# Kernel tuning notes

Hardware: AMD Instinct MI355X
Metric: run time of the kernel (lower is better)

## Reference

```python
import jax, jax.numpy as jnp
import numpy as np

EPS = 1e-10
PHI = (1.0 + np.sqrt(5.0)) / 2.0
TAU = 2.0 * np.pi
LOG_CUTOFF = float(np.log(PHI ** 2))  # log(lambda_cutoff)


def _log_abs_diff(la, lb, same_sign):
    # log|a - b| (same sign) or log(|a| + |b|) (opposite sign), all in log space
    hi = jnp.maximum(la, lb)
    lo = jnp.minimum(la, lb)
    d = jnp.minimum(lo - hi, -1e-7)  # guard log1p(-1) on the (masked) diagonal
    log_diff = hi + jnp.log1p(-jnp.exp(d))
    log_sum = jnp.logaddexp(la, lb)
    return jnp.where(same_sign, log_diff, log_sum)


def log_cartesian_distance(ell1, theta1, ell2, theta2):
    # elementwise / broadcasting version of compute_log_cartesian_distance
    cos1, sin1 = jnp.cos(theta1), jnp.sin(theta1)
    cos2, sin2 = jnp.cos(theta2), jnp.sin(theta2)
    lx1 = ell1 + jnp.log(jnp.abs(cos1) + EPS)
    ly1 = ell1 + jnp.log(jnp.abs(sin1) + EPS)
    lx2 = ell2 + jnp.log(jnp.abs(cos2) + EPS)
    ly2 = ell2 + jnp.log(jnp.abs(sin2) + EPS)
    same_x = (jnp.sign(cos1) * jnp.sign(cos2)) > 0
    same_y = (jnp.sign(sin1) * jnp.sign(sin2)) > 0
    ldx = _log_abs_diff(lx1, lx2, same_x)
    ldy = _log_abs_diff(ly1, ly2, same_y)
    # 0.5 * logsumexp(2*ldx, 2*ldy) == log sqrt(dx^2 + dy^2)
    return 0.5 * jnp.logaddexp(2.0 * ldx, 2.0 * ldy)


def setup_inputs() -> dict:
    N = 4096
    key = jax.random.key(0)
    k1, k2 = jax.random.split(key)
    ell = jax.random.uniform(k1, (N,), dtype=jnp.float32) * np.float32(np.log(PHI ** 3))
    theta = jax.random.uniform(k2, (N,), dtype=jnp.float32) * np.float32(TAU)
    s = jnp.ones((N,), dtype=jnp.float32)
    frozen = jnp.zeros((N,), dtype=bool)
    return {"ell": ell, "theta": theta, "s": s, "frozen": frozen}


def reference(ell, theta, s, frozen):
    # compute_repulsion_direct: all-pairs log-distance repulsion with phi^2 cutoff
    N = ell.shape[0]
    # pairwise log distances: [N, N]
    ld = log_cartesian_distance(ell[:, None], theta[:, None], ell[None, :], theta[None, :])
    pair_mask = (ld <= LOG_CUTOFF) & (~jnp.eye(N, dtype=bool)) & (~frozen)[:, None]
    force = s[:, None] * s[None, :] * jnp.exp(-ld)  # s_i * s_j / dist
    force = jnp.where(pair_mask, force, jnp.zeros((), force.dtype))
    d_theta = jnp.mod(theta[None, :] - theta[:, None] + np.float32(np.pi), np.float32(TAU)) - np.float32(np.pi)
    d_ell = ell[None, :] - ell[:, None]
    F_ell = jnp.sum(force * d_ell, axis=1)
    F_theta = jnp.sum(force * d_theta, axis=1)
    return jnp.stack([F_ell, F_theta])  # [2, N]
```

## Files before the change

kernel.cpp:

```cpp
#include <hip/hip_runtime.h>
#include <math.h>

#define BLOCK 256
#define IPB 4

#define PI_F      3.14159265358979323846f
#define TAU_F     6.2831853071795864769f
#define INV_TAU_F 0.15915494309189533577f
#define PHI4_F    6.854101966249685f

extern "C" __device__ float __builtin_amdgcn_rsqf(float);

__global__ __launch_bounds__(BLOCK) void repulse_fused(
        const float* __restrict__ ell,
        const float* __restrict__ theta,
        const float* __restrict__ s,
        const unsigned char* __restrict__ frozen,
        float* __restrict__ out, int n) {
    const int t  = threadIdx.x;
    const int i0 = blockIdx.x * IPB;

    float xi[IPB], yi[IPB], eli[IPB], api[IPB];
#pragma unroll
    for (int v = 0; v < IPB; ++v) {
        int i = i0 + v;
        float e  = ell[i];
        float th = theta[i];
        float lam = __expf(e);
        float sn, cs;
        __sincosf(th, &sn, &cs);
        xi[v] = lam * cs; yi[v] = lam * sn;
        eli[v] = e;
        api[v] = PI_F - th;
    }

    float Fe[IPB], Ft[IPB];
#pragma unroll
    for (int v = 0; v < IPB; ++v) { Fe[v] = 0.0f; Ft[v] = 0.0f; }

#pragma unroll 4
    for (int j = t; j < n; j += BLOCK) {
        float e  = ell[j];
        float th = theta[j];
        float sj = s[j];
        float lam = __expf(e);
        float sn, cs;
        __sincosf(th, &sn, &cs);
        float bx = lam * cs, by = lam * sn;
#pragma unroll
        for (int v = 0; v < IPB; ++v) {
            float dx = bx - xi[v];
            float dy = by - yi[v];
            float r2 = fmaf(dx, dx, dy * dy);
            float rinv = __builtin_amdgcn_rsqf(r2);
            bool ok = (r2 <= PHI4_F) && (r2 > 0.0f);
            float f = ok ? sj * rinv : 0.0f;
            float tt = th + api[v];
            float dth = fmaf(-floorf(tt * INV_TAU_F), TAU_F, tt) - PI_F;
            Fe[v] = fmaf(f, e - eli[v], Fe[v]);
            Ft[v] = fmaf(f, dth, Ft[v]);
        }
    }

#pragma unroll
    for (int v = 0; v < IPB; ++v) {
#pragma unroll
        for (int off = 32; off >= 1; off >>= 1) {
            Fe[v] += __shfl_xor(Fe[v], off, 64);
            Ft[v] += __shfl_xor(Ft[v], off, 64);
        }
    }

    __shared__ float red[(BLOCK / 64) * IPB * 2];
    const int wave = t >> 6;
    const int lane = t & 63;
    if (lane == 0) {
#pragma unroll
        for (int v = 0; v < IPB; ++v) {
            red[wave * IPB * 2 + v * 2 + 0] = Fe[v];
            red[wave * IPB * 2 + v * 2 + 1] = Ft[v];
        }
    }
    __syncthreads();

    if (t < IPB * 2) {
        int v = t >> 1;
        int c = t & 1;
        float sum = 0.0f;
#pragma unroll
        for (int w = 0; w < BLOCK / 64; ++w)
            sum += red[w * IPB * 2 + v * 2 + c];
        int i = i0 + v;
        float val = frozen[i] ? 0.0f : s[i] * sum;
        out[c * n + i] = val;
    }
}

extern "C" void kernel_launch(void* const* d_in, const int* in_sizes, int n_in,
                              void* d_out, int out_size, void* d_ws, size_t ws_size,
                              hipStream_t stream) {
    const float* ell   = (const float*)d_in[0];
    const float* theta = (const float*)d_in[1];
    const float* s     = (const float*)d_in[2];
    const unsigned char* frozen = (const unsigned char*)d_in[3];
    float* out = (float*)d_out;
    int n = in_sizes[0];

    int grid = (n + IPB - 1) / IPB;
    repulse_fused<<<grid, BLOCK, 0, stream>>>(ell, theta, s, frozen, out, n);
}
```

Baseline: 68.90 us.

## Precompute per-point Cartesian coordinates in a separate kernel before pair loop

Adds a prepass kernel that computes exp(ell)*cos/sin(theta) once per point and packs x, y, ell and theta into a float4 workspace array. The main all-pairs kernel then loads one float4 per j instead of recomputing exp and sincos for every (block, j) pair. This removes redundant transcendental work from the inner loop. In exchange it adds a second kernel launch and an extra global write and read of the packed array.

New measurement: 69.87 us. No clear change (+1.4%).

```diff
diff --git a/kernel.cpp b/kernel.cpp
--- a/kernel.cpp
+++ b/kernel.cpp
@@ -11,9 +11,23 @@
 
 extern "C" __device__ float __builtin_amdgcn_rsqf(float);
 
-__global__ __launch_bounds__(BLOCK) void repulse_fused(
+__global__ __launch_bounds__(256) void precompute_xy(
         const float* __restrict__ ell,
         const float* __restrict__ theta,
+        float4* __restrict__ P, int n) {
+    int j = blockIdx.x * 256 + threadIdx.x;
+    if (j < n) {
+        float e  = ell[j];
+        float th = theta[j];
+        float lam = __expf(e);
+        float sn, cs;
+        __sincosf(th, &sn, &cs);
+        P[j] = make_float4(lam * cs, lam * sn, e, th);
+    }
+}
+
+__global__ __launch_bounds__(BLOCK) void repulse_main(
+        const float4* __restrict__ P,
         const float* __restrict__ s,
         const unsigned char* __restrict__ frozen,
         float* __restrict__ out, int n) {
@@ -23,15 +37,11 @@
     float xi[IPB], yi[IPB], eli[IPB], api[IPB];
 #pragma unroll
     for (int v = 0; v < IPB; ++v) {
-        int i = i0 + v;
-        float e  = ell[i];
-        float th = theta[i];
-        float lam = __expf(e);
-        float sn, cs;
-        __sincosf(th, &sn, &cs);
-        xi[v] = lam * cs; yi[v] = lam * sn;
-        eli[v] = e;
-        api[v] = PI_F - th;
+        float4 pi = P[i0 + v];
+        xi[v]  = pi.x;
+        yi[v]  = pi.y;
+        eli[v] = pi.z;
+        api[v] = PI_F - pi.w;
     }
 
     float Fe[IPB], Ft[IPB];
@@ -40,24 +50,19 @@
 
 #pragma unroll 4
     for (int j = t; j < n; j += BLOCK) {
-        float e  = ell[j];
-        float th = theta[j];
-        float sj = s[j];
-        float lam = __expf(e);
-        float sn, cs;
-        __sincosf(th, &sn, &cs);
-        float bx = lam * cs, by = lam * sn;
+        float4 p  = P[j];
+        float  sj = s[j];
 #pragma unroll
         for (int v = 0; v < IPB; ++v) {
-            float dx = bx - xi[v];
-            float dy = by - yi[v];
+            float dx = p.x - xi[v];
+            float dy = p.y - yi[v];
             float r2 = fmaf(dx, dx, dy * dy);
             float rinv = __builtin_amdgcn_rsqf(r2);
             bool ok = (r2 <= PHI4_F) && (r2 > 0.0f);
             float f = ok ? sj * rinv : 0.0f;
-            float tt = th + api[v];
+            float tt = p.w + api[v];
             float dth = fmaf(-floorf(tt * INV_TAU_F), TAU_F, tt) - PI_F;
-            Fe[v] = fmaf(f, e - eli[v], Fe[v]);
+            Fe[v] = fmaf(f, p.z - eli[v], Fe[v]);
             Ft[v] = fmaf(f, dth, Ft[v]);
         }
     }
@@ -106,6 +111,10 @@
     float* out = (float*)d_out;
     int n = in_sizes[0];
 
+    float4* P = (float4*)d_ws;
+
+    precompute_xy<<<(n + 255) / 256, 256, 0, stream>>>(ell, theta, P, n);
+
     int grid = (n + IPB - 1) / IPB;
-    repulse_fused<<<grid, BLOCK, 0, stream>>>(ell, theta, s, frozen, out, n);
+    repulse_main<<<grid, BLOCK, 0, stream>>>(P, s, frozen, out, n);
 }
```
